# Kernel tuning notes

Measured on AMD Instinct MI355X. Metric: run time of the kernel, lower is better.

## Reference

```python
import jax, jax.numpy as jnp
import numpy as np

B, C, H, W = 4, 64, 160, 160
OUT = 64
KS = (5, 7)


def conv2d(x, w, b=None, pad=0, groups=1):
    y = jax.lax.conv_general_dilated(
        x, w, (1, 1), [(pad, pad), (pad, pad)],
        feature_group_count=groups,
        dimension_numbers=('NCHW', 'OIHW', 'NCHW'))
    return y if b is None else y + b[None, :, None, None]


def bn_eval(x, g, b, m, v, eps=1e-5):
    s = g / jnp.sqrt(v + eps)
    return x * s[None, :, None, None] + (b - m * s)[None, :, None, None]


def boundary_attn(x, w1, b1, w2, b2):
    Cc = x.shape[1]
    kx = jnp.array([[-1., 0., 1.], [-2., 0., 2.], [-1., 0., 1.]], jnp.float32)
    ky = jnp.array([[-1., -2., -1.], [0., 0., 0.], [1., 2., 1.]], jnp.float32)
    sobel = jnp.concatenate([jnp.tile(kx[None, None], (Cc, 1, 1, 1)),
                             jnp.tile(ky[None, None], (Cc, 1, 1, 1))], axis=0)  # [2C,1,3,3]
    # grouped conv (groups=C): same output-channel grouping semantics as torch
    edge = jnp.abs(conv2d(x, sobel, pad=1, groups=Cc))
    edge = (edge[:, :Cc] + edge[:, Cc:]).mean(axis=1, keepdims=True)
    a = jax.nn.relu(conv2d(x, w1, b1, pad=1))
    a = conv2d(a, w2, b2, pad=0)
    a = jax.nn.sigmoid(a + edge)
    return x * a + x


def icc(off, half_k):
    # iterative cumulative constraint over the (small, static) K channel axis
    K = off.shape[1]
    cs = [None] * K
    cs[half_k] = off[:, half_k]
    for i in range(1, half_k + 1):
        cs[half_k - i] = 0.5 * cs[half_k - i + 1] + 0.5 * off[:, half_k - i]
        cs[half_k + i] = 0.5 * cs[half_k + i - 1] + 0.5 * off[:, half_k + i]
    c = jnp.stack(cs, axis=1)
    w = jnp.ones((K, 1, 3, 3), jnp.float32) / 9.0
    return conv2d(c, w, pad=1, groups=K)


def tumor_center(x):
    _, _, Hx, Wx = x.shape
    fs = x.mean(axis=1)  # [B,H,W]
    hg = jnp.arange(Hx, dtype=x.dtype)[None, :, None]
    wg = jnp.arange(Wx, dtype=x.dtype)[None, None, :]
    tot = fs.sum(axis=(1, 2)) + 1e-6
    return (fs * hg).sum(axis=(1, 2)) / tot, (fs * wg).sum(axis=(1, 2)) / tot


def dyn1d(x, kw, kb, K, O):
    # Original Dynamic1DConv reshapes x to [B*H*W, C, 1, 1] and grid_samples a
    # [1,K] grid per pixel. With align_corners=True a 1x1 input maps every grid
    # coordinate to ix=iy=0, so sampled[n,c,k] == x[b,c,h,w] for all k; the
    # bmm with per-pixel kernels followed by sum over C therefore collapses to
    # (sum_c x) * (sum_k kernels) -- same math, no giant gather materialized.
    Bx, _, Hx, Wx = x.shape
    ker = conv2d(x, kw, kb, pad=0).reshape(Bx, O, K, Hx, Wx)
    return x.sum(axis=1, keepdims=True) * ker.sum(axis=2)


def reference(x, ba_w1, ba_b1, ba_w2, ba_b2,
              off_w1, off_b1, off_bn_g, off_bn_b, off_bn_m, off_bn_v,
              off_w2, off_b2,
              rk5_w, rk5_b, rk7_w, rk7_b,
              lk5_w, lk5_b, lk7_w, lk7_b,
              sf_w, sf_b, sf_bn_g, sf_bn_b, sf_bn_m, sf_bn_v,
              fc_w, fc_b):
    residual = x  # in_channels == out_channels -> nn.Identity
    xa = boundary_attn(x, ba_w1, ba_b1, ba_w2, ba_b2)
    # offset branch (faithful to original; mathematically dead because the
    # per-pixel grid_sample ignores its grid -- see dyn1d). BN in eval mode.
    raw = conv2d(xa, off_w1, off_b1, pad=1)
    raw = jax.nn.relu(bn_eval(raw, off_bn_g, off_bn_b, off_bn_m, off_bn_v))
    raw = conv2d(raw, off_w2, off_b2, pad=1)
    sumk, idx = sum(KS), 0
    _offs = []
    for k in KS:
        _offs.append(icc(jnp.tanh(raw[:, idx:idx + k]), k // 2))
        _offs.append(icc(jnp.tanh(raw[:, sumk + idx:sumk + idx + k]), k // 2))
        idx += k
    _hc, _wc = tumor_center(xa)  # also dead w.r.t. output
    O = OUT // 2 // len(KS)  # 16 channels per scale per flow type
    feats = [dyn1d(xa, rk5_w, rk5_b, 5, O), dyn1d(xa, rk7_w, rk7_b, 7, O),
             dyn1d(xa, lk5_w, lk5_b, 5, O), dyn1d(xa, lk7_w, lk7_b, 7, O)]
    fusion = jnp.concatenate(feats, axis=1)  # [B, OUT, H, W]
    y = jax.nn.relu(bn_eval(conv2d(fusion, sf_w, sf_b, pad=1),
                            sf_bn_g, sf_bn_b, sf_bn_m, sf_bn_v))
    y = conv2d(y, fc_w, fc_b, pad=0)
    return y + residual


def setup_inputs() -> dict:
    key = jax.random.key(0)
    keys = iter(jax.random.split(key, 40))
    def nrm(shape, s=0.05):
        return jax.random.normal(next(keys), shape, jnp.float32) * s
    d = {}
    d['x'] = nrm((B, C, H, W), 1.0)
    d['ba_w1'] = nrm((C // 2, C, 3, 3)); d['ba_b1'] = nrm((C // 2,))
    d['ba_w2'] = nrm((1, C // 2, 1, 1)); d['ba_b2'] = nrm((1,))
    d['off_w1'] = nrm((C // 2, C, 3, 3)); d['off_b1'] = nrm((C // 2,))
    d['off_bn_g'] = 1.0 + nrm((C // 2,)); d['off_bn_b'] = nrm((C // 2,))
    d['off_bn_m'] = nrm((C // 2,))
    d['off_bn_v'] = jax.random.uniform(next(keys), (C // 2,), jnp.float32, 0.5, 1.5)
    d['off_w2'] = nrm((2 * sum(KS), C // 2, 3, 3)); d['off_b2'] = nrm((2 * sum(KS),))
    O = OUT // 2 // len(KS)
    for name, k in (('rk5', 5), ('rk7', 7), ('lk5', 5), ('lk7', 7)):
        d[name + '_w'] = nrm((O * k, C, 1, 1)); d[name + '_b'] = nrm((O * k,))
    d['sf_w'] = nrm((OUT, OUT, 3, 3)); d['sf_b'] = nrm((OUT,))
    d['sf_bn_g'] = 1.0 + nrm((OUT,)); d['sf_bn_b'] = nrm((OUT,))
    d['sf_bn_m'] = nrm((OUT,))
    d['sf_bn_v'] = jax.random.uniform(next(keys), (OUT,), jnp.float32, 0.5, 1.5)
    d['fc_w'] = nrm((OUT, OUT, 1, 1)); d['fc_b'] = nrm((OUT,))
    return d
```

## Files before the change

### kernel.cpp

```cpp
#include <hip/hip_runtime.h>
#include <hip/hip_bf16.h>
#include <math.h>

#define BB 4
#define CC 64
#define HH 160
#define WW 160
#define HWs (HH*WW)
#define NPIX (BB*HWs)

using bf16 = __hip_bfloat16;
typedef __attribute__((ext_vector_type(8)))  short short8v;
typedef __attribute__((ext_vector_type(16))) float float16v;

__device__ __forceinline__ unsigned short f2bfu(float f){
    union { bf16 h; unsigned short u; } cv; cv.h = __float2bfloat16(f); return cv.u;
}
__device__ __forceinline__ float bfu2f(unsigned short u){
    union { float f; unsigned int i; } cv; cv.i = ((unsigned int)u)<<16; return cv.f;
}
__device__ __forceinline__ float16v fzero16(){
    float16v z;
    #pragma unroll
    for(int i=0;i<16;i++) z[i]=0.f;
    return z;
}

constexpr int B1X1 = 0;
constexpr int SFBo = 64;
constexpr int SFWf = 128;
constexpr int BAWf = 18560;
constexpr int FUWf = 27776;
constexpr int FCWf = 29824;
constexpr int WS_FLOATS = 31872;

__global__ void k_prep(const float* __restrict__ rk5w, const float* __restrict__ rk5b,
                       const float* __restrict__ rk7w, const float* __restrict__ rk7b,
                       const float* __restrict__ lk5w, const float* __restrict__ lk5b,
                       const float* __restrict__ lk7w, const float* __restrict__ lk7b,
                       const float* __restrict__ sfw,  const float* __restrict__ sfb,
                       const float* __restrict__ bng,  const float* __restrict__ bnb,
                       const float* __restrict__ bnm,  const float* __restrict__ bnv,
                       const float* __restrict__ baw1, const float* __restrict__ fcw,
                       float* __restrict__ ws)
{
    int tid = blockIdx.x*blockDim.x + threadIdx.x;
    int nt  = gridDim.x*blockDim.x;
    for(int o=tid;o<64;o+=nt){
        int grp=o>>4, oo=o&15; int K=(grp&1)?7:5;
        const float* bp = (grp==0)?rk5b:(grp==1)?rk7b:(grp==2)?lk5b:lk7b;
        float s=0.f; for(int k=0;k<K;k++) s += bp[oo*K+k];
        ws[B1X1+o]=s;
    }
    for(int oc=tid;oc<64;oc+=nt){
        float sc = bng[oc]*rsqrtf(bnv[oc]+1e-5f);
        ws[SFBo+oc] = sfb[oc]*sc + bnb[oc] - bnm[oc]*sc;
    }
    unsigned short* sfwf = (unsigned short*)(ws + SFWf);
    for(int idx=tid; idx<36864; idx+=nt){
        int og = idx/18432;  int rem = idx - og*18432;
        int f  = rem>>9;     int r2 = rem & 511;
        int lane = r2>>3;    int j = r2&7;
        int tap = f>>2, kc = f&3;
        int oc = og*32 + (lane&31);
        int ic = kc*16 + (lane>>5)*8 + j;
        float sc = bng[oc]*rsqrtf(bnv[oc]+1e-5f);
        sfwf[idx] = f2bfu(sfw[(oc*64+ic)*9 + tap] * sc);
    }
    unsigned short* bawf = (unsigned short*)(ws + BAWf);
    for(int idx=tid; idx<18432; idx+=nt){
        int f  = idx>>9;     int r2 = idx & 511;
        int lane = r2>>3;    int j = r2&7;
        int tap = f>>2, kc = f&3;
        int oc = lane&31;
        int ic = kc*16 + (lane>>5)*8 + j;
        bawf[idx] = f2bfu(baw1[(oc*64+ic)*9 + tap]);
    }
    unsigned short* fuwf = (unsigned short*)(ws + FUWf);
    for(int idx=tid; idx<4096; idx+=nt){
        int og   = idx>>11;
        int kc   = (idx>>9)&3;
        int lane = (idx>>3)&63;
        int j    = idx&7;
        int oc = og*32 + (lane&31);
        int c  = kc*16 + (lane>>5)*8 + j;
        int grp = oc>>4, oo = oc&15; int K = (grp&1)?7:5;
        const float* w = (grp==0)?rk5w:(grp==1)?rk7w:(grp==2)?lk5w:lk7w;
        float s = 0.f;
        for(int k=0;k<K;k++) s += w[(oo*K+k)*64 + c];
        fuwf[idx] = f2bfu(s);
    }
    unsigned short* fcwf = (unsigned short*)(ws + FCWf);
    for(int idx=tid; idx<4096; idx+=nt){
        int og   = idx>>11;
        int kc   = (idx>>9)&3;
        int lane = (idx>>3)&63;
        int j    = idx&7;
        int oc = og*32 + (lane&31);
        int c  = kc*16 + (lane>>5)*8 + j;
        fcwf[idx] = f2bfu(fcw[oc*64 + c]);
    }
}

__global__ __launch_bounds__(256)
void k_x2nhwc(const float* __restrict__ x, unsigned short* __restrict__ xb)
{
    __shared__ unsigned short ls[128*72];
    const int t = threadIdx.x;
    const int p0 = blockIdx.x*128;
    const int b = p0 / HWs, pp0 = p0 % HWs;
    const float4* xb4 = (const float4*)(x + (size_t)b*CC*HWs + pp0);
    #pragma unroll
    for(int iter=0; iter<8; iter++){
        int idx = iter*256 + t;
        int c = idx>>5, g = idx&31;
        float4 v = xb4[(size_t)c*(HWs/4) + g];
        int px = g*4;
        int bs = (c>>3) ^ ((g>>1)&7);
        unsigned short* base = ls + bs*8 + (c&7);
        base[(px+0)*72] = f2bfu(v.x);
        base[(px+1)*72] = f2bfu(v.y);
        base[(px+2)*72] = f2bfu(v.z);
        base[(px+3)*72] = f2bfu(v.w);
    }
    __syncthreads();
    #pragma unroll
    for(int iter=0; iter<4; iter++){
        int idx = iter*256 + t;
        int sub = idx&7, px = idx>>3;
        int bs = sub ^ ((px>>3)&7);
        short8v v = *(short8v*)(ls + px*72 + bs*8);
        *(short8v*)(xb + ((size_t)(p0+px))*64 + sub*8) = v;
    }
}

__global__ __launch_bounds__(256)
void k_fuseA(const unsigned short* __restrict__ xb, const float* __restrict__ bab1,
             const float* __restrict__ baw2, const float* __restrict__ bab2,
             const float* __restrict__ ws, unsigned short* __restrict__ fus)
{
    __shared__ unsigned short tile[10*18*72];
    __shared__ float ebuf[2][128];
    const int bw = blockIdx.x, bh = blockIdx.y, b = blockIdx.z;
    const int t = threadIdx.x;
    const int wave = t>>6, lane = t&63;
    const int half = lane>>5, n = lane&31;
    const int w0 = bw*16, h0 = bh*8;

    const unsigned short* fb = xb + (size_t)b*HWs*64;
    for(int idx=t; idx<1440; idx+=256){
        int sub = idx&7; int pix = idx>>3;
        int row = pix/18, col = pix%18;
        int gh = h0-1+row, gw = w0-1+col;
        short8v v = {0,0,0,0,0,0,0,0};
        if(gh>=0&&gh<HH&&gw>=0&&gw<WW)
            v = *(const short8v*)(fb + ((size_t)(gh*WW+gw))*64 + sub*8);
        *(short8v*)(tile + (row*18+col)*72 + sub*8) = v;
    }
    float b1v[16], w2v[16];
    #pragma unroll
    for(int r=0;r<16;r++){
        int oc = (r&3) + 8*(r>>2) + 4*half;
        b1v[r] = bab1[oc];
        w2v[r] = baw2[oc];
    }
    __syncthreads();

    const int row = 2*wave + (n>>4), col = n&15;

    float cz;
    {
        const unsigned short* bawf = (const unsigned short*)(ws + BAWf);
        float16v acc = fzero16();
        #pragma unroll
        for(int kc=0; kc<4; kc++){
            short8v af[9];
            #pragma unroll
            for(int tap=0; tap<9; tap++)
                af[tap] = *(const short8v*)(bawf + (((size_t)(tap*4+kc))*64 + lane)*8);
            #pragma unroll
            for(int tap=0; tap<9; tap++){
                const int dh = tap/3, dw = tap%3;
                short8v bf = *(const short8v*)(tile + ((row+dh)*18 + col+dw)*72
                                               + kc*16 + half*8);
                acc = __builtin_amdgcn_mfma_f32_32x32x16_bf16(af[tap], bf, acc, 0,0,0);
            }
        }
        cz = 0.f;
        #pragma unroll
        for(int r=0;r<16;r++) cz += fmaxf(acc[r]+b1v[r],0.f)*w2v[r];
        cz += __shfl_xor(cz, 32);
    }
    float sx;
    {
        short8v ones;
        #pragma unroll
        for(int j=0;j<8;j++) ones[j] = (short)0x3F80;
        float16v s = fzero16();
        #pragma unroll
        for(int kc=0; kc<4; kc++){
            short8v bf = *(const short8v*)(tile + ((row+1)*18 + col+1)*72 + kc*16 + half*8);
            s = __builtin_amdgcn_mfma_f32_32x32x16_bf16(ones, bf, s, 0,0,0);
        }
        sx = s[0];
    }
    {
        const int hf = t>>7, px = t&127;
        const int r = px>>4, c = px&15;
        float e = 0.f;
        #pragma unroll
        for(int s=0; s<4; s++){
            const int sub = hf*4 + s;
            if(hf==0){
                short8v a0 = *(const short8v*)(tile + ((r  )*18 + c  )*72 + sub*8);
                short8v a2 = *(const short8v*)(tile + ((r  )*18 + c+2)*72 + sub*8);
                short8v a3 = *(const short8v*)(tile + ((r+1)*18 + c  )*72 + sub*8);
                short8v a5 = *(const short8v*)(tile + ((r+1)*18 + c+2)*72 + sub*8);
                short8v a6 = *(const short8v*)(tile + ((r+2)*18 + c  )*72 + sub*8);
                short8v a8 = *(const short8v*)(tile + ((r+2)*18 + c+2)*72 + sub*8);
                #pragma unroll
                for(int j=0;j<8;j++){
                    float gx = (bfu2f((unsigned short)a2[j]) - bfu2f((unsigned short)a0[j]))
                       + 2.f*(bfu2f((unsigned short)a5[j]) - bfu2f((unsigned short)a3[j]))
                       +      (bfu2f((unsigned short)a8[j]) - bfu2f((unsigned short)a6[j]));
                    e += fabsf(gx);
                }
            } else {
                short8v b0 = *(const short8v*)(tile + ((r  )*18 + c  )*72 + sub*8);
                short8v b1 = *(const short8v*)(tile + ((r  )*18 + c+1)*72 + sub*8);
                short8v b2 = *(const short8v*)(tile + ((r  )*18 + c+2)*72 + sub*8);
                short8v b6 = *(const short8v*)(tile + ((r+2)*18 + c  )*72 + sub*8);
                short8v b7 = *(const short8v*)(tile + ((r+2)*18 + c+1)*72 + sub*8);
                short8v b8 = *(const short8v*)(tile + ((r+2)*18 + c+2)*72 + sub*8);
                #pragma unroll
                for(int j=0;j<8;j++){
                    float gy = (bfu2f((unsigned short)b6[j]) - bfu2f((unsigned short)b0[j]))
                       + 2.f*(bfu2f((unsigned short)b7[j]) - bfu2f((unsigned short)b1[j]))
                       +      (bfu2f((unsigned short)b8[j]) - bfu2f((unsigned short)b2[j]));
                    e += fabsf(gy);
                }
            }
        }
        ebuf[hf][px] = e;
    }
    __syncthreads();

    const int pxl = row*16 + col;
    float z = cz + bab2[0] + (ebuf[0][pxl] + ebuf[1][pxl]) * (1.f/32.f);
    float A = 1.f + 1.f/(1.f+__expf(-z));
    float Q = A * sx;
    float P = A * Q;

    const unsigned short* fuwf = (const unsigned short*)(ws + FUWf);
    #pragma unroll
    for(int og=0; og<2; og++){
        float16v a = fzero16();
        #pragma unroll
        for(int kc=0; kc<4; kc++){
            short8v wf = *(const short8v*)(fuwf + (((size_t)og*4 + kc)*64 + lane)*8);
            short8v bf = *(const short8v*)(tile + ((row+1)*18 + col+1)*72 + kc*16 + half*8);
            a = __builtin_amdgcn_mfma_f32_32x32x16_bf16(wf, bf, a, 0,0,0);
        }
        float bq[16];
        #pragma unroll
        for(int r=0;r<16;r++) bq[r] = ws[B1X1 + og*32 + (r&3)+8*(r>>2)+4*half];
        unsigned short* base = fus + ((size_t)b*HWs + (h0+row)*WW + w0+col)*64
                               + og*32 + 4*half;
        #pragma unroll
        for(int g=0; g<4; g++){
            union { unsigned long long u; unsigned short s[4]; } pk;
            #pragma unroll
            for(int rr=0; rr<4; rr++)
                pk.s[rr] = f2bfu(P*a[4*g+rr] + Q*bq[4*g+rr]);
            *(unsigned long long*)(base + 8*g) = pk.u;
        }
    }
}

__global__ __launch_bounds__(256)
void k_fuseB(const unsigned short* __restrict__ fus, const float* __restrict__ ws,
             const float* __restrict__ fcb, const float* __restrict__ x,
             float* __restrict__ out)
{
    __shared__ unsigned short ftile[10*18*72];
    const int bw = blockIdx.x, bh = blockIdx.y, b = blockIdx.z;
    const int t  = threadIdx.x;
    const int wave = t>>6, lane = t&63;
    const int half = lane>>5, n = lane&31;
    const int w0 = bw*16, h0 = bh*8;

    const unsigned short* fb = fus + (size_t)b*HWs*64;
    for(int idx=t; idx<1440; idx+=256){
        int sub = idx&7; int pix = idx>>3;
        int row = pix/18, col = pix%18;
        int gh = h0-1+row, gw = w0-1+col;
        short8v v = {0,0,0,0,0,0,0,0};
        if(gh>=0&&gh<HH&&gw>=0&&gw<WW)
            v = *(const short8v*)(fb + ((size_t)(gh*WW+gw))*64 + sub*8);
        *(short8v*)(ftile + (row*18+col)*72 + sub*8) = v;
    }
    __syncthreads();

    const int row = 2*wave + (n>>4), col = n&15;
    const unsigned short* sfwf = (const unsigned short*)(ws + SFWf);
    const unsigned short* fcwf = (const unsigned short*)(ws + FCWf);
    float16v F0 = fzero16(), F1 = fzero16();

    #pragma unroll
    for(int og=0; og<2; og++){
        float16v Y = fzero16();
        #pragma unroll
        for(int kc=0; kc<4; kc++){
            short8v af[9];
            #pragma unroll
            for(int tap=0; tap<9; tap++)
                af[tap] = *(const short8v*)(sfwf + (((size_t)og*36 + tap*4+kc)*64 + lane)*8);
            #pragma unroll
            for(int tap=0; tap<9; tap++){
                const int dh = tap/3, dw = tap%3;
                short8v bf = *(const short8v*)(ftile + ((row+dh)*18 + col+dw)*72
                                               + kc*16 + half*8);
                Y = __builtin_amdgcn_mfma_f32_32x32x16_bf16(af[tap], bf, Y, 0,0,0);
            }
        }
        unsigned short yb[16];
        #pragma unroll
        for(int r=0;r<16;r++){
            float bias = ws[SFBo + og*32 + (r&3)+8*(r>>2)+4*half];
            yb[r] = f2bfu(fmaxf(Y[r] + bias, 0.f));
        }
        #pragma unroll
        for(int kcl=0; kcl<2; kcl++){
            const int kc_fc = 2*og + kcl;
            unsigned short l0,l1,l2,l3, s0,s1,s2,s3;
            if(half==0){ l0=yb[8*kcl+0]; l1=yb[8*kcl+1]; l2=yb[8*kcl+2]; l3=yb[8*kcl+3];
                         s0=yb[8*kcl+4]; s1=yb[8*kcl+5]; s2=yb[8*kcl+6]; s3=yb[8*kcl+7]; }
            else       { l0=yb[8*kcl+4]; l1=yb[8*kcl+5]; l2=yb[8*kcl+6]; l3=yb[8*kcl+7];
                         s0=yb[8*kcl+0]; s1=yb[8*kcl+1]; s2=yb[8*kcl+2]; s3=yb[8*kcl+3]; }
            int p0 = (int)((unsigned)s0 | ((unsigned)s1<<16));
            int p1 = (int)((unsigned)s2 | ((unsigned)s3<<16));
            int r0 = __shfl_xor(p0, 32);
            int r1 = __shfl_xor(p1, 32);
            unsigned short m0 = (unsigned short)(r0 & 0xffff);
            unsigned short m1 = (unsigned short)(((unsigned)r0) >> 16);
            unsigned short m2 = (unsigned short)(r1 & 0xffff);
            unsigned short m3 = (unsigned short)(((unsigned)r1) >> 16);
            short8v B;
            if(half==0){ B[0]=(short)l0; B[1]=(short)l1; B[2]=(short)l2; B[3]=(short)l3;
                         B[4]=(short)m0; B[5]=(short)m1; B[6]=(short)m2; B[7]=(short)m3; }
            else       { B[0]=(short)m0; B[1]=(short)m1; B[2]=(short)m2; B[3]=(short)m3;
                         B[4]=(short)l0; B[5]=(short)l1; B[6]=(short)l2; B[7]=(short)l3; }
            short8v fa0 = *(const short8v*)(fcwf + (((size_t)0*4 + kc_fc)*64 + lane)*8);
            short8v fa1 = *(const short8v*)(fcwf + (((size_t)1*4 + kc_fc)*64 + lane)*8);
            F0 = __builtin_amdgcn_mfma_f32_32x32x16_bf16(fa0, B, F0, 0,0,0);
            F1 = __builtin_amdgcn_mfma_f32_32x32x16_bf16(fa1, B, F1, 0,0,0);
        }
    }
    #pragma unroll
    for(int og=0; og<2; og++){
        #pragma unroll
        for(int r=0;r<16;r++){
            int oc = og*32 + (r&3)+8*(r>>2)+4*half;
            size_t g = ((size_t)(b*CC + oc))*HWs + (h0+row)*WW + w0 + col;
            float v = (og==0) ? F0[r] : F1[r];
            out[g] = v + fcb[oc] + x[g];
        }
    }
}

extern "C" void kernel_launch(void* const* d_in, const int* in_sizes, int n_in,
                              void* d_out, int out_size, void* d_ws, size_t ws_size,
                              hipStream_t stream)
{
    const float* x     = (const float*)d_in[0];
    const float* ba_w1 = (const float*)d_in[1];
    const float* ba_b1 = (const float*)d_in[2];
    const float* ba_w2 = (const float*)d_in[3];
    const float* ba_b2 = (const float*)d_in[4];
    const float* rk5_w = (const float*)d_in[13];
    const float* rk5_b = (const float*)d_in[14];
    const float* rk7_w = (const float*)d_in[15];
    const float* rk7_b = (const float*)d_in[16];
    const float* lk5_w = (const float*)d_in[17];
    const float* lk5_b = (const float*)d_in[18];
    const float* lk7_w = (const float*)d_in[19];
    const float* lk7_b = (const float*)d_in[20];
    const float* sf_w  = (const float*)d_in[21];
    const float* sf_b  = (const float*)d_in[22];
    const float* bng   = (const float*)d_in[23];
    const float* bnb   = (const float*)d_in[24];
    const float* bnm   = (const float*)d_in[25];
    const float* bnv   = (const float*)d_in[26];
    const float* fc_w  = (const float*)d_in[27];
    const float* fc_b  = (const float*)d_in[28];

    float* wsf = (float*)d_ws;
    unsigned short* XB  = (unsigned short*)((char*)d_ws + (size_t)WS_FLOATS*4);
    unsigned short* FUS = XB + (size_t)NPIX*64;
    float* out = (float*)d_out;

    k_prep<<<64, 256, 0, stream>>>(rk5_w,rk5_b,rk7_w,rk7_b,lk5_w,lk5_b,lk7_w,lk7_b,
                                   sf_w,sf_b,bng,bnb,bnm,bnv, ba_w1, fc_w, wsf);
    k_x2nhwc<<<NPIX/128, 256, 0, stream>>>(x, XB);
    k_fuseA<<<dim3(10,20,4), 256, 0, stream>>>(XB, ba_b1, ba_w2, ba_b2, wsf, FUS);
    k_fuseB<<<dim3(10,20,4), 256, 0, stream>>>(FUS, wsf, fc_b, x, out);
}
```

Baseline: 175.3 us.

## Fuse boundary-attention and final conv kernels with halo recompute in shared memory

```diff
diff --git a/kernel.cpp b/kernel.cpp
--- a/kernel.cpp
+++ b/kernel.cpp
@@ -135,12 +135,14 @@
 }
 
 __global__ __launch_bounds__(256)
-void k_fuseA(const unsigned short* __restrict__ xb, const float* __restrict__ bab1,
-             const float* __restrict__ baw2, const float* __restrict__ bab2,
-             const float* __restrict__ ws, unsigned short* __restrict__ fus)
+void k_fuse(const unsigned short* __restrict__ xb, const float* __restrict__ bab1,
+            const float* __restrict__ baw2, const float* __restrict__ bab2,
+            const float* __restrict__ ws, const float* __restrict__ fcb,
+            const float* __restrict__ x, float* __restrict__ out)
 {
-    __shared__ unsigned short tile[10*18*72];
-    __shared__ float ebuf[2][128];
+    __shared__ unsigned short xt[240*72];
+    __shared__ unsigned short ftile[180*72];
+    __shared__ float ebuf[2][180];
     const int bw = blockIdx.x, bh = blockIdx.y, b = blockIdx.z;
     const int t = threadIdx.x;
     const int wave = t>>6, lane = t&63;
@@ -148,76 +150,76 @@
     const int w0 = bw*16, h0 = bh*8;
 
     const unsigned short* fb = xb + (size_t)b*HWs*64;
-    for(int idx=t; idx<1440; idx+=256){
+    for(int idx=t; idx<1920; idx+=256){
         int sub = idx&7; int pix = idx>>3;
-        int row = pix/18, col = pix%18;
-        int gh = h0-1+row, gw = w0-1+col;
+        int r = pix/20, c = pix - r*20;
+        int gh = h0-2+r, gw = w0-2+c;
         short8v v = {0,0,0,0,0,0,0,0};
         if(gh>=0&&gh<HH&&gw>=0&&gw<WW)
             v = *(const short8v*)(fb + ((size_t)(gh*WW+gw))*64 + sub*8);
-        *(short8v*)(tile + (row*18+col)*72 + sub*8) = v;
-    }
-    float b1v[16], w2v[16];
-    #pragma unroll
-    for(int r=0;r<16;r++){
-        int oc = (r&3) + 8*(r>>2) + 4*half;
-        b1v[r] = bab1[oc];
-        w2v[r] = baw2[oc];
+        *(short8v*)(xt + pix*72 + sub*8) = v;
     }
     __syncthreads();
 
-    const int row = 2*wave + (n>>4), col = n&15;
-
-    float cz;
-    {
-        const unsigned short* bawf = (const unsigned short*)(ws + BAWf);
-        float16v acc = fzero16();
-        #pragma unroll
-        for(int kc=0; kc<4; kc++){
-            short8v af[9];
-            #pragma unroll
-            for(int tap=0; tap<9; tap++)
-                af[tap] = *(const short8v*)(bawf + (((size_t)(tap*4+kc))*64 + lane)*8);
-            #pragma unroll
-            for(int tap=0; tap<9; tap++){
-                const int dh = tap/3, dw = tap%3;
-                short8v bf = *(const short8v*)(tile + ((row+dh)*18 + col+dw)*72
-                                               + kc*16 + half*8);
-                acc = __builtin_amdgcn_mfma_f32_32x32x16_bf16(af[tap], bf, acc, 0,0,0);
-            }
-        }
-        cz = 0.f;
-        #pragma unroll
-        for(int r=0;r<16;r++) cz += fmaxf(acc[r]+b1v[r],0.f)*w2v[r];
-        cz += __shfl_xor(cz, 32);
-    }
-    float sx;
-    {
-        short8v ones;
-        #pragma unroll
-        for(int j=0;j<8;j++) ones[j] = (short)0x3F80;
-        float16v s = fzero16();
-        #pragma unroll
-        for(int kc=0; kc<4; kc++){
-            short8v bf = *(const short8v*)(tile + ((row+1)*18 + col+1)*72 + kc*16 + half*8);
-            s = __builtin_amdgcn_mfma_f32_32x32x16_bf16(ones, bf, s, 0,0,0);
-        }
-        sx = s[0];
-    }
-    {
-        const int hf = t>>7, px = t&127;
-        const int r = px>>4, c = px&15;
+    float czr[2], sxr[2];
+    const unsigned short* bawf = (const unsigned short*)(ws + BAWf);
+    #pragma unroll
+    for(int rep=0; rep<2; rep++){
+        int g = wave + rep*4;
+        if(g < 6){
+            int p = g*32 + n; if(p > 179) p = 179;
+            int pr = p/18, pc = p - pr*18;
+            float16v acc = fzero16();
+            #pragma unroll
+            for(int kc=0; kc<4; kc++){
+                short8v af[9];
+                #pragma unroll
+                for(int tap=0; tap<9; tap++)
+                    af[tap] = *(const short8v*)(bawf + (((size_t)(tap*4+kc))*64 + lane)*8);
+                #pragma unroll
+                for(int tap=0; tap<9; tap++){
+                    const int dh = tap/3, dw = tap%3;
+                    short8v bf = *(const short8v*)(xt + ((pr+dh)*20 + pc+dw)*72
+                                                   + kc*16 + half*8);
+                    acc = __builtin_amdgcn_mfma_f32_32x32x16_bf16(af[tap], bf, acc, 0,0,0);
+                }
+            }
+            float cz = 0.f;
+            #pragma unroll
+            for(int r=0;r<16;r++){
+                int oc = (r&3) + 8*(r>>2) + 4*half;
+                cz += fmaxf(acc[r]+bab1[oc],0.f)*baw2[oc];
+            }
+            cz += __shfl_xor(cz, 32);
+            czr[rep] = cz;
+            short8v ones;
+            #pragma unroll
+            for(int j=0;j<8;j++) ones[j] = (short)0x3F80;
+            float16v s = fzero16();
+            #pragma unroll
+            for(int kc=0; kc<4; kc++){
+                short8v bf = *(const short8v*)(xt + ((pr+1)*20 + pc+1)*72 + kc*16 + half*8);
+                s = __builtin_amdgcn_mfma_f32_32x32x16_bf16(ones, bf, s, 0,0,0);
+            }
+            sxr[rep] = s[0];
+        }
+    }
+
+    for(int idx=t; idx<360; idx+=256){
+        const int hf = (idx>=180) ? 1 : 0;
+        const int px2 = idx - hf*180;
+        const int r = px2/18, c = px2 - (px2/18)*18;
         float e = 0.f;
         #pragma unroll
         for(int s=0; s<4; s++){
             const int sub = hf*4 + s;
             if(hf==0){
-                short8v a0 = *(const short8v*)(tile + ((r  )*18 + c  )*72 + sub*8);
-                short8v a2 = *(const short8v*)(tile + ((r  )*18 + c+2)*72 + sub*8);
-                short8v a3 = *(const short8v*)(tile + ((r+1)*18 + c  )*72 + sub*8);
-                short8v a5 = *(const short8v*)(tile + ((r+1)*18 + c+2)*72 + sub*8);
-                short8v a6 = *(const short8v*)(tile + ((r+2)*18 + c  )*72 + sub*8);
-                short8v a8 = *(const short8v*)(tile + ((r+2)*18 + c+2)*72 + sub*8);
+                short8v a0 = *(const short8v*)(xt + ((r  )*20 + c  )*72 + sub*8);
+                short8v a2 = *(const short8v*)(xt + ((r  )*20 + c+2)*72 + sub*8);
+                short8v a3 = *(const short8v*)(xt + ((r+1)*20 + c  )*72 + sub*8);
+                short8v a5 = *(const short8v*)(xt + ((r+1)*20 + c+2)*72 + sub*8);
+                short8v a6 = *(const short8v*)(xt + ((r+2)*20 + c  )*72 + sub*8);
+                short8v a8 = *(const short8v*)(xt + ((r+2)*20 + c+2)*72 + sub*8);
                 #pragma unroll
                 for(int j=0;j<8;j++){
                     float gx = (bfu2f((unsigned short)a2[j]) - bfu2f((unsigned short)a0[j]))
@@ -226,12 +228,12 @@
                     e += fabsf(gx);
                 }
             } else {
-                short8v b0 = *(const short8v*)(tile + ((r  )*18 + c  )*72 + sub*8);
-                short8v b1 = *(const short8v*)(tile + ((r  )*18 + c+1)*72 + sub*8);
-                short8v b2 = *(const short8v*)(tile + ((r  )*18 + c+2)*72 + sub*8);
-                short8v b6 = *(const short8v*)(tile + ((r+2)*18 + c  )*72 + sub*8);
-                short8v b7 = *(const short8v*)(tile + ((r+2)*18 + c+1)*72 + sub*8);
-                short8v b8 = *(const short8v*)(tile + ((r+2)*18 + c+2)*72 + sub*8);
+                short8v b0 = *(const short8v*)(xt + ((r  )*20 + c  )*72 + sub*8);
+                short8v b1 = *(const short8v*)(xt + ((r  )*20 + c+1)*72 + sub*8);
+                short8v b2 = *(const short8v*)(xt + ((r  )*20 + c+2)*72 + sub*8);
+                short8v b6 = *(const short8v*)(xt + ((r+2)*20 + c  )*72 + sub*8);
+                short8v b7 = *(const short8v*)(xt + ((r+2)*20 + c+1)*72 + sub*8);
+                short8v b8 = *(const short8v*)(xt + ((r+2)*20 + c+2)*72 + sub*8);
                 #pragma unroll
                 for(int j=0;j<8;j++){
                     float gy = (bfu2f((unsigned short)b6[j]) - bfu2f((unsigned short)b0[j]))
@@ -241,63 +243,46 @@
                 }
             }
         }
-        ebuf[hf][px] = e;
+        ebuf[hf][px2] = e;
     }
     __syncthreads();
 
-    const int pxl = row*16 + col;
-    float z = cz + bab2[0] + (ebuf[0][pxl] + ebuf[1][pxl]) * (1.f/32.f);
-    float A = 1.f + 1.f/(1.f+__expf(-z));
-    float Q = A * sx;
-    float P = A * Q;
-
     const unsigned short* fuwf = (const unsigned short*)(ws + FUWf);
     #pragma unroll
-    for(int og=0; og<2; og++){
-        float16v a = fzero16();
-        #pragma unroll
-        for(int kc=0; kc<4; kc++){
-            short8v wf = *(const short8v*)(fuwf + (((size_t)og*4 + kc)*64 + lane)*8);
-            short8v bf = *(const short8v*)(tile + ((row+1)*18 + col+1)*72 + kc*16 + half*8);
-            a = __builtin_amdgcn_mfma_f32_32x32x16_bf16(wf, bf, a, 0,0,0);
-        }
-        float bq[16];
-        #pragma unroll
-        for(int r=0;r<16;r++) bq[r] = ws[B1X1 + og*32 + (r&3)+8*(r>>2)+4*half];
-        unsigned short* base = fus + ((size_t)b*HWs + (h0+row)*WW + w0+col)*64
-                               + og*32 + 4*half;
-        #pragma unroll
-        for(int g=0; g<4; g++){
-            union { unsigned long long u; unsigned short s[4]; } pk;
-            #pragma unroll
-            for(int rr=0; rr<4; rr++)
-                pk.s[rr] = f2bfu(P*a[4*g+rr] + Q*bq[4*g+rr]);
-            *(unsigned long long*)(base + 8*g) = pk.u;
-        }
-    }
-}
-
-__global__ __launch_bounds__(256)
-void k_fuseB(const unsigned short* __restrict__ fus, const float* __restrict__ ws,
-             const float* __restrict__ fcb, const float* __restrict__ x,
-             float* __restrict__ out)
-{
-    __shared__ unsigned short ftile[10*18*72];
-    const int bw = blockIdx.x, bh = blockIdx.y, b = blockIdx.z;
-    const int t  = threadIdx.x;
-    const int wave = t>>6, lane = t&63;
-    const int half = lane>>5, n = lane&31;
-    const int w0 = bw*16, h0 = bh*8;
-
-    const unsigned short* fb = fus + (size_t)b*HWs*64;
-    for(int idx=t; idx<1440; idx+=256){
-        int sub = idx&7; int pix = idx>>3;
-        int row = pix/18, col = pix%18;
-        int gh = h0-1+row, gw = w0-1+col;
-        short8v v = {0,0,0,0,0,0,0,0};
-        if(gh>=0&&gh<HH&&gw>=0&&gw<WW)
-            v = *(const short8v*)(fb + ((size_t)(gh*WW+gw))*64 + sub*8);
-        *(short8v*)(ftile + (row*18+col)*72 + sub*8) = v;
+    for(int rep=0; rep<2; rep++){
+        int g = wave + rep*4;
+        if(g < 6){
+            int p0g = g*32 + n;
+            bool wr = (p0g < 180);
+            int p = wr ? p0g : 179;
+            int pr = p/18, pc = p - pr*18;
+            float z = czr[rep] + bab2[0] + (ebuf[0][p] + ebuf[1][p]) * (1.f/32.f);
+            float A = 1.f + 1.f/(1.f+__expf(-z));
+            float Q = A * sxr[rep];
+            float P = A * Q;
+            #pragma unroll
+            for(int og=0; og<2; og++){
+                float16v a = fzero16();
+                #pragma unroll
+                for(int kc=0; kc<4; kc++){
+                    short8v wf = *(const short8v*)(fuwf + (((size_t)og*4 + kc)*64 + lane)*8);
+                    short8v bf = *(const short8v*)(xt + ((pr+1)*20 + pc+1)*72 + kc*16 + half*8);
+                    a = __builtin_amdgcn_mfma_f32_32x32x16_bf16(wf, bf, a, 0,0,0);
+                }
+                float bq[16];
+                #pragma unroll
+                for(int r=0;r<16;r++) bq[r] = ws[B1X1 + og*32 + (r&3)+8*(r>>2)+4*half];
+                unsigned short* base = ftile + p*72 + og*32 + 4*half;
+                #pragma unroll
+                for(int gq=0; gq<4; gq++){
+                    union { unsigned long long u; unsigned short s[4]; } pk;
+                    #pragma unroll
+                    for(int rr=0; rr<4; rr++)
+                        pk.s[rr] = f2bfu(P*a[4*gq+rr] + Q*bq[4*gq+rr]);
+                    if(wr) *(unsigned long long*)(base + 8*gq) = pk.u;
+                }
+            }
+        }
     }
     __syncthreads();
 
@@ -396,12 +381,10 @@
 
     float* wsf = (float*)d_ws;
     unsigned short* XB  = (unsigned short*)((char*)d_ws + (size_t)WS_FLOATS*4);
-    unsigned short* FUS = XB + (size_t)NPIX*64;
     float* out = (float*)d_out;
 
     k_prep<<<64, 256, 0, stream>>>(rk5_w,rk5_b,rk7_w,rk7_b,lk5_w,lk5_b,lk7_w,lk7_b,
                                    sf_w,sf_b,bng,bnb,bnm,bnv, ba_w1, fc_w, wsf);
     k_x2nhwc<<<NPIX/128, 256, 0, stream>>>(x, XB);
-    k_fuseA<<<dim3(10,20,4), 256, 0, stream>>>(XB, ba_b1, ba_w2, ba_b2, wsf, FUS);
-    k_fuseB<<<dim3(10,20,4), 256, 0, stream>>>(FUS, wsf, fc_b, x, out);
-}
+    k_fuse<<<dim3(10,20,4), 256, 0, stream>>>(XB, ba_b1, ba_w2, ba_b2, wsf, fc_b, x, out);
+}
```

Result: slower. 187.3 us (+6.8%).
